# Performance work log

Measured on AMD Instinct MI355X. Metric: run time of the kernel, lower is better.

## Reference

```python
import jax, jax.numpy as jnp
from jax import lax
import numpy as np

T, B, D, H = 4096, 32, 512, 256


def setup_inputs() -> dict:
    key = jax.random.key(0)
    ks = jax.random.split(key, 8)
    s_ih = 1.0 / np.sqrt(H)
    inp = {
        "x": jax.random.normal(ks[0], (T, B, D), dtype=jnp.float32),
        "reset": jax.random.randint(ks[1], (T, B), 0, 2, dtype=jnp.int32),
        # PyTorch nn.LSTM params, gate order (i, f, g, o)
        "W_ih": jax.random.uniform(ks[2], (4 * H, D), jnp.float32, -s_ih, s_ih),
        "W_hh": jax.random.uniform(ks[3], (4 * H, H), jnp.float32, -s_ih, s_ih),
        "b_ih": jax.random.uniform(ks[4], (4 * H,), jnp.float32, -s_ih, s_ih),
        "b_hh": jax.random.uniform(ks[5], (4 * H,), jnp.float32, -s_ih, s_ih),
        "W_proj": jax.random.uniform(ks[6], (1, H), jnp.float32, -s_ih, s_ih),
        "b_proj": jax.random.uniform(ks[7], (1,), jnp.float32, -s_ih, s_ih),
    }
    return inp


def _lstm_with_reset(x, reset, W_ih, W_hh, b_ih, b_hh):
    # Precompute input contribution for all timesteps: [T, B, 4H]
    xW = jnp.einsum("tbd,gd->tbg", x, W_ih) + b_ih + b_hh
    h0 = jnp.zeros((x.shape[1], H), x.dtype)
    c0 = jnp.zeros((x.shape[1], H), x.dtype)

    def step(carry, inp):
        h, c = carry
        xw, r = inp
        keep = (1 - r).astype(h.dtype)[:, None]  # zero state at episode starts
        h = h * keep
        c = c * keep
        gates = xw + h @ W_hh.T  # [B, 4H]
        i, f, g, o = jnp.split(gates, 4, axis=-1)
        c = jax.nn.sigmoid(f) * c + jax.nn.sigmoid(i) * jnp.tanh(g)
        h = jax.nn.sigmoid(o) * jnp.tanh(c)
        return (h, c), h

    (_, _), hs = lax.scan(step, (h0, c0), (xW, reset))
    return hs  # [T, B, H]


def reference(x, reset, W_ih, W_hh, b_ih, b_hh, W_proj, b_proj):
    hs = _lstm_with_reset(x, reset, W_ih, W_hh, b_ih, b_hh)
    return hs @ W_proj.T + b_proj  # [T, B, 1]
```

## Files before the change

### kernel.cpp

```cpp
#include <hip/hip_runtime.h>
#include <cstdint>
#include <cstddef>

#define T_DIM 4096
#define B_DIM 32
#define D_DIM 512
#define H_DIM 256
#define G_DIM 1024
#define HSTR 264
#define XSTR 1036
#define NBUCK 64

typedef _Float16 h8 __attribute__((ext_vector_type(8)));
typedef float f4 __attribute__((ext_vector_type(4)));

__global__ void seg_build_kernel(const int* __restrict__ reset,
                                 unsigned* __restrict__ starts,
                                 unsigned* __restrict__ segcnt) {
  __shared__ unsigned cnts[256];
  __shared__ unsigned offs[256];
  const int b = blockIdx.x;
  const int tid = threadIdx.x;
  const int t0 = tid * 16;
  unsigned c = 0;
  for (int e = 0; e < 16; ++e) {
    int t = t0 + e;
    bool pred = (t == 0) || (reset[t * B_DIM + b] != 0);
    c += pred ? 1u : 0u;
  }
  cnts[tid] = c;
  __syncthreads();
  if (tid == 0) {
    unsigned run = 0;
    for (int i = 0; i < 256; ++i) { unsigned v = cnts[i]; offs[i] = run; run += v; }
    segcnt[b] = run;
  }
  __syncthreads();
  unsigned o = (unsigned)b * 4096u + offs[tid];
  for (int e = 0; e < 16; ++e) {
    int t = t0 + e;
    bool pred = (t == 0) || (reset[t * B_DIM + b] != 0);
    if (pred) { starts[o++] = (unsigned)t; }
  }
}

__global__ void seg_flat_kernel(const unsigned* __restrict__ starts,
                                const unsigned* __restrict__ segcnt,
                                uint2* __restrict__ flat2,
                                unsigned* __restrict__ meta) {
  __shared__ unsigned offs;
  const int b = blockIdx.x;
  const int tid = threadIdx.x;
  if (tid == 0) {
    unsigned o = 0;
    for (int i = 0; i < b; ++i) o += segcnt[i];
    offs = o;
    if (b == 31) meta[1] = o + segcnt[31];
    if (b == 0) meta[0] = 0u;
  }
  __syncthreads();
  const unsigned cnt = segcnt[b];
  const unsigned off = offs;
  for (unsigned s = tid; s < cnt; s += 256) {
    unsigned t0 = starts[b * 4096u + s];
    unsigned t1 = (s + 1 < cnt) ? starts[b * 4096u + s + 1] : 4096u;
    flat2[off + s] = make_uint2(t0 | ((unsigned)b << 16), t1);
  }
}

__global__ void seg_sort_kernel(const uint2* __restrict__ flat2,
                                uint2* __restrict__ flat,
                                const unsigned* __restrict__ meta) {
  __shared__ unsigned lh[NBUCK];
  __shared__ unsigned cur[NBUCK];
  const unsigned nseg = meta[1];
  const int tid = threadIdx.x;
  const int lane = tid & 63;
  if (tid < NBUCK) lh[tid] = 0u;
  __syncthreads();
  for (unsigned base = 0; base < nseg; base += 1024) {
    unsigned i = base + tid;
    bool act = i < nseg;
    unsigned bk = 0u;
    if (act) {
      uint2 e = flat2[i];
      bk = min(e.y - (e.x & 0xFFFFu), (unsigned)NBUCK) - 1u;
    }
    unsigned long long rem = __ballot(act);
    while (rem) {
      int ld = (int)__ffsll((unsigned long long)rem) - 1;
      unsigned lbk = __shfl(bk, ld);
      unsigned long long meq = __ballot(act && bk == lbk);
      if (lane == ld) atomicAdd(&lh[lbk], (unsigned)__popcll(meq));
      rem &= ~meq;
    }
  }
  __syncthreads();
  if (tid == 0) {
    unsigned run = 0;
    for (int k = NBUCK - 1; k >= 0; --k) { cur[k] = run; run += lh[k]; }
  }
  __syncthreads();
  for (unsigned base = 0; base < nseg; base += 1024) {
    unsigned i = base + tid;
    bool act = i < nseg;
    uint2 e = make_uint2(0u, 0u);
    unsigned bk = 0u;
    if (act) {
      e = flat2[i];
      bk = min(e.y - (e.x & 0xFFFFu), (unsigned)NBUCK) - 1u;
    }
    unsigned long long rem = __ballot(act);
    unsigned pos = 0u;
    while (rem) {
      int ld = (int)__ffsll((unsigned long long)rem) - 1;
      unsigned lbk = __shfl(bk, ld);
      unsigned long long meq = __ballot(act && bk == lbk);
      unsigned bs = 0u;
      if (lane == ld) bs = atomicAdd(&cur[lbk], (unsigned)__popcll(meq));
      bs = __shfl(bs, ld);
      if (act && bk == lbk)
        pos = bs + (unsigned)__popcll(meq & ((1ull << lane) - 1ull));
      rem &= ~meq;
    }
    if (act) flat[pos] = e;
  }
}

__global__ void wpack_kernel(const float* __restrict__ Whh,
                             _Float16* __restrict__ wpack) {
  int gid = blockIdx.x * 256 + threadIdx.x;
  int nt = gid >> 9;
  int rem = gid & 511;
  int ks = rem >> 6;
  int l = rem & 63;
  int n = nt * 16 + (l & 15);
  int k = ks * 32 + (l >> 4) * 8;
  const float* src = Whh + (size_t)n * H_DIM + k;
  f4 v0 = *(const f4*)src;
  f4 v1 = *(const f4*)(src + 4);
  h8 wv = {(_Float16)v0.x, (_Float16)v0.y, (_Float16)v0.z, (_Float16)v0.w,
           (_Float16)v1.x, (_Float16)v1.y, (_Float16)v1.z, (_Float16)v1.w};
  *(h8*)(wpack + (size_t)gid * 8) = wv;
}

#define BM 128
#define BN 128
#define BK 32

__global__ __launch_bounds__(256) void xw_gemm_kernel(
    const float* __restrict__ X, const float* __restrict__ Wih,
    const float* __restrict__ bih, const float* __restrict__ bhh,
    _Float16* __restrict__ xw) {
  __shared__ _Float16 As[BM * BK];
  __shared__ _Float16 Bs[BN * BK];
  const int tid = threadIdx.x;
  const int lane = tid & 63;
  const int wave = tid >> 6;
  const unsigned wg = blockIdx.x;
  const unsigned xcd = wg & 7u;
  const unsigned idx = wg >> 3;
  const size_t m0 = (size_t)(xcd * 128u + (idx >> 3)) * BM;
  const int n0 = (int)(idx & 7u) * BN;
  const int wm = (wave & 1) * 64;
  const int wn = (wave >> 1) * 64;
  const int q = lane >> 4;
  const int r = lane & 15;

  f4 acc[4][4];
#pragma unroll
  for (int i = 0; i < 4; ++i)
#pragma unroll
    for (int j = 0; j < 4; ++j) { f4 z = {0.f, 0.f, 0.f, 0.f}; acc[i][j] = z; }

  const int srow = tid >> 1;
  const int kh = (tid & 1) * 16;

  for (int k0 = 0; k0 < D_DIM; k0 += BK) {
    const float* ax = X + (m0 + (size_t)srow) * D_DIM + k0 + kh;
    const float* bx = Wih + ((size_t)(n0 + srow)) * D_DIM + k0 + kh;
    f4 a0 = *(const f4*)(ax);
    f4 a1 = *(const f4*)(ax + 4);
    f4 a2 = *(const f4*)(ax + 8);
    f4 a3 = *(const f4*)(ax + 12);
    f4 b0 = *(const f4*)(bx);
    f4 b1 = *(const f4*)(bx + 4);
    f4 b2 = *(const f4*)(bx + 8);
    f4 b3 = *(const f4*)(bx + 12);
    h8 ha0 = {(_Float16)a0.x, (_Float16)a0.y, (_Float16)a0.z, (_Float16)a0.w,
              (_Float16)a1.x, (_Float16)a1.y, (_Float16)a1.z, (_Float16)a1.w};
    h8 ha1 = {(_Float16)a2.x, (_Float16)a2.y, (_Float16)a2.z, (_Float16)a2.w,
              (_Float16)a3.x, (_Float16)a3.y, (_Float16)a3.z, (_Float16)a3.w};
    h8 hb0 = {(_Float16)b0.x, (_Float16)b0.y, (_Float16)b0.z, (_Float16)b0.w,
              (_Float16)b1.x, (_Float16)b1.y, (_Float16)b1.z, (_Float16)b1.w};
    h8 hb1 = {(_Float16)b2.x, (_Float16)b2.y, (_Float16)b2.z, (_Float16)b2.w,
              (_Float16)b3.x, (_Float16)b3.y, (_Float16)b3.z, (_Float16)b3.w};
    *(h8*)(As + srow * BK + kh) = ha0;
    *(h8*)(As + srow * BK + kh + 8) = ha1;
    *(h8*)(Bs + srow * BK + kh) = hb0;
    *(h8*)(Bs + srow * BK + kh + 8) = hb1;
    __syncthreads();

    h8 af[4], bf[4];
#pragma unroll
    for (int mi = 0; mi < 4; ++mi)
      af[mi] = *(const h8*)(As + (wm + mi * 16 + r) * BK + q * 8);
#pragma unroll
    for (int ni = 0; ni < 4; ++ni)
      bf[ni] = *(const h8*)(Bs + (wn + ni * 16 + r) * BK + q * 8);
#pragma unroll
    for (int mi = 0; mi < 4; ++mi)
#pragma unroll
      for (int ni = 0; ni < 4; ++ni)
        acc[mi][ni] = __builtin_amdgcn_mfma_f32_16x16x32_f16(af[mi], bf[ni], acc[mi][ni], 0, 0, 0);
    __syncthreads();
  }

#pragma unroll
  for (int mi = 0; mi < 4; ++mi) {
#pragma unroll
    for (int ni = 0; ni < 4; ++ni) {
      int n = n0 + wn + ni * 16 + r;
      float bias = bih[n] + bhh[n];
#pragma unroll
      for (int reg = 0; reg < 4; ++reg) {
        size_t m = m0 + (size_t)(wm + mi * 16 + q * 4 + reg);
        xw[m * G_DIM + n] = (_Float16)(acc[mi][ni][reg] + bias);
      }
    }
  }
}

__device__ __forceinline__ float sigmf(float x) {
  return __builtin_amdgcn_rcpf(1.f + __expf(-x));
}
__device__ __forceinline__ float tanhf_(float x) {
  return 2.f * __builtin_amdgcn_rcpf(1.f + __expf(-2.f * x)) - 1.f;
}
__device__ __forceinline__ f4 MF(h8 a, h8 b, f4 c) {
  return __builtin_amdgcn_mfma_f32_16x16x32_f16(a, b, c, 0, 0, 0);
}

#define WPKp(g, j, ks) \
  ((const h8*)(wpack + (((size_t)((((g)*16 + 2*w + (j)) * 8 + (ks))) * 64 + l) * 8)))
#define ARD(mt, ks) (*(const h8*)(Hbuf + (16*(mt) + r16) * HSTR + (ks)*32 + q*8))

#define MFK_REG(KS) do {                                                   \
  h8 a0_ = ARD(0, KS), a1_ = ARD(1, KS);                                   \
  _Pragma("unroll") for (int g = 0; g < 4; ++g)                            \
  _Pragma("unroll") for (int j = 0; j < 2; ++j) {                          \
    acc[0][g][j] = MF(a0_, wr[g][j][KS], acc[0][g][j]);                    \
    acc[1][g][j] = MF(a1_, wr[g][j][KS], acc[1][g][j]); }                  \
} while (0)

#define MFK_W2() do {                                                      \
  h8 a0_ = ARD(0, 2), a1_ = ARD(1, 2);                                     \
  _Pragma("unroll") for (int g = 0; g < 4; ++g)                            \
  _Pragma("unroll") for (int j = 0; j < 2; ++j) {                          \
    h8 b_ = *(const h8*)(Wlds + (size_t)((((g)*16 + 2*w + (j)) * 64 + l)) * 8); \
    acc[0][g][j] = MF(a0_, b_, acc[0][g][j]);                              \
    acc[1][g][j] = MF(a1_, b_, acc[1][g][j]); }                            \
} while (0)

#define MFK_S(BUF, KS) do {                                                \
  h8 a0_ = ARD(0, KS), a1_ = ARD(1, KS);                                   \
  _Pragma("unroll") for (int g = 0; g < 4; ++g)                            \
  _Pragma("unroll") for (int j = 0; j < 2; ++j) {                          \
    acc[0][g][j] = MF(a0_, BUF[g][j], acc[0][g][j]);                       \
    acc[1][g][j] = MF(a1_, BUF[g][j], acc[1][g][j]); }                     \
} while (0)

#define LOAD_S(BUF, KS) do {                                               \
  _Pragma("unroll") for (int g = 0; g < 4; ++g)                            \
  _Pragma("unroll") for (int j = 0; j < 2; ++j)                            \
    BUF[g][j] = *WPKp(g, j, KS);                                           \
} while (0)

#define XRD(MT, G, J) do {                                                 \
  f4 xv;                                                                   \
  int rb_ = 16*(MT) + q*4;                                                 \
  int nn_ = (G)*256 + w*32 + 16*(J) + r16;                                 \
  xv.x = (float)xwlds[(rb_+0)*XSTR + nn_];                                 \
  xv.y = (float)xwlds[(rb_+1)*XSTR + nn_];                                 \
  xv.z = (float)xwlds[(rb_+2)*XSTR + nn_];                                 \
  xv.w = (float)xwlds[(rb_+3)*XSTR + nn_];                                 \
  acc[MT][G][J] += xv; } while (0)

#define CONTROL_STEP do {                                                     \
  int m = tid;                                                                \
  bool aliv = alivef[m] != 0;                                                 \
  if (aliv) {                                                                 \
    unsigned oi = outix[m];                                                   \
    if (oi != 0xFFFFFFFFu) {                                                  \
      float s = bp;                                                           \
      _Pragma("unroll") for (int ww = 0; ww < 8; ++ww) s += pbuf[ww][m];      \
      __builtin_nontemporal_store(s, &out[oi]);                               \
    }                                                                         \
  }                                                                           \
  bool cont = aliv && (tcur[m] + 1 < tend[m]);                                \
  bool need = aliv && !cont;                                                  \
  unsigned long long bal = __ballot(need);                                    \
  if (cont) {                                                                 \
    int t = tcur[m] + 1;                                                      \
    tcur[m] = t; keepm[m] = 1.f;                                              \
    unsigned row = (unsigned)t * 32u + (unsigned)bcol[m];                     \
    trowB[m] = row * 2048u; outix[m] = row;                                   \
  }                                                                           \
  if (bal) {                                                                  \
    unsigned cntp = (unsigned)__popcll(bal);                                  \
    int ldr = (int)__ffsll(bal) - 1;                                          \
    unsigned basep = 0;                                                       \
    if ((tid & 63) == ldr) basep = atomicAdd(ctr, cntp);                      \
    basep = __shfl(basep, ldr);                                               \
    if (need) {                                                               \
      unsigned idx = basep +                                                  \
          (unsigned)__popcll(bal & ((1ull << (tid & 63)) - 1ull));            \
      if (idx < nseg) {                                                       \
        uint2 sg = flat[idx];                                                 \
        int t0s = (int)(sg.x & 0xFFFFu); int bb = (int)(sg.x >> 16);          \
        tcur[m] = t0s; tend[m] = (int)sg.y; bcol[m] = bb; keepm[m] = 0.f;     \
        unsigned row = (unsigned)t0s * 32u + (unsigned)bb;                    \
        trowB[m] = row * 2048u; outix[m] = row;                               \
        h8 zz = {0,0,0,0,0,0,0,0};                                            \
        _Pragma("unroll") for (int i2 = 0; i2 < 33; ++i2)                     \
          *(h8*)(Hbuf + (size_t)m * HSTR + i2 * 8) = zz;                      \
      } else {                                                                \
        alivef[m] = 0; outix[m] = 0xFFFFFFFFu; trowB[m] = 0;                  \
        keepm[m] = 0.f;                                                       \
      }                                                                       \
    }                                                                         \
  }                                                                           \
} while (0)

__global__ __launch_bounds__(512, 2) void lstm_scan_mfma(
    const _Float16* __restrict__ xw,
    const _Float16* __restrict__ wpack,
    const float* __restrict__ Wproj,
    const float* __restrict__ bproj,
    const uint2* __restrict__ flat,
    unsigned* __restrict__ meta,
    float* __restrict__ out) {
  __shared__ __align__(16) _Float16 Wlds[64 * 64 * 8];
  __shared__ __align__(16) _Float16 xwlds[32 * XSTR];
  __shared__ __align__(16) _Float16 Hbuf[32 * HSTR];
  __shared__ __align__(16) float pbuf[8][32];
  __shared__ __align__(16) unsigned trowB[32];
  __shared__ __align__(16) float keepm[32];
  __shared__ unsigned outix[32];
  __shared__ int tcur[32], tend[32], bcol[32], alivef[32];

  const int tid = threadIdx.x;
  const int l = tid & 63;
  const int w = tid >> 6;
  const int q = l >> 4;
  const int r16 = l & 15;
  const char* xwc = (const char*)xw;
  unsigned* ctr = meta;
  const unsigned nseg = meta[1];

  for (int it = 0; it < 16; ++it) {
    int idx = it * 512 + tid;
    int nt = idx >> 6;
    int ll = idx & 63;
    *(h8*)(Wlds + (size_t)idx * 8) =
        *(const h8*)(wpack + (((size_t)(nt * 8 + 2)) * 64 + ll) * 8);
  }
  for (int i = tid; i < 32 * HSTR / 8; i += 512) {
    h8 z = {0,0,0,0,0,0,0,0};
    *(h8*)(Hbuf + (size_t)i * 8) = z;
  }
  h8 wr[4][2][2];
#pragma unroll
  for (int g = 0; g < 4; ++g)
#pragma unroll
    for (int j = 0; j < 2; ++j)
#pragma unroll
      for (int ks = 0; ks < 2; ++ks)
        wr[g][j][ks] = *WPKp(g, j, ks);

  const float wpv0 = Wproj[32 * w + r16];
  const float wpv1 = Wproj[32 * w + 16 + r16];
  const float bp = bproj[0];
  if (tid < 32) {
    alivef[tid] = 1; tcur[tid] = 0; tend[tid] = 0; bcol[tid] = 0;
    outix[tid] = 0xFFFFFFFFu; trowB[tid] = 0; keepm[tid] = 0.f;
  }
  float cst[16];
#pragma unroll
  for (int i = 0; i < 16; ++i) cst[i] = 0.f;
  __syncthreads();
  if (tid < 32) CONTROL_STEP;
  int nalive = __syncthreads_count(tid < 32 ? alivef[tid] : 0);

  while (nalive > 0) {
#pragma unroll
    for (int rnd = 0; rnd < 8; ++rnd) {
      int c = rnd * 8 + w;
      unsigned rowB = trowB[c >> 1];
      const char* src = xwc + (size_t)rowB + (size_t)((c & 1) * 1024) + (size_t)l * 16;
      _Float16* dst = xwlds + (size_t)(c >> 1) * XSTR + (c & 1) * 512;
      __builtin_amdgcn_global_load_lds((const uint32_t*)src, (uint32_t*)dst, 16, 0, 0);
    }

    f4 z4 = {0.f, 0.f, 0.f, 0.f};
    f4 acc[2][4][2];
#pragma unroll
    for (int mt = 0; mt < 2; ++mt)
#pragma unroll
      for (int g = 0; g < 4; ++g)
#pragma unroll
        for (int j = 0; j < 2; ++j) acc[mt][g][j] = z4;
    h8 sA[4][2], sB[4][2];

    LOAD_S(sA, 3); LOAD_S(sB, 4);
    MFK_REG(0);
    MFK_REG(1);
    MFK_W2();
    MFK_S(sA, 3); LOAD_S(sA, 5);
    MFK_S(sB, 4); LOAD_S(sB, 6);
    MFK_S(sA, 5); LOAD_S(sA, 7);
    MFK_S(sB, 6);
    MFK_S(sA, 7);

    __syncthreads();

    XRD(0, 0, 0); XRD(0, 0, 1);
    XRD(0, 1, 0); XRD(0, 1, 1);
    XRD(0, 2, 0); XRD(0, 2, 1);
    XRD(0, 3, 0); XRD(0, 3, 1);
    XRD(1, 0, 0); XRD(1, 0, 1);
    XRD(1, 1, 0); XRD(1, 1, 1);
    XRD(1, 2, 0); XRD(1, 2, 1);
    XRD(1, 3, 0); XRD(1, 3, 1);

    f4 kp0 = *(const f4*)&keepm[q * 4];
    f4 kp1 = *(const f4*)&keepm[16 + q * 4];
    float pr[8];
#pragma unroll
    for (int r = 0; r < 4; ++r) {
      {
        float gi = sigmf(acc[0][0][0][r]);
        float gf = sigmf(acc[0][1][0][r]);
        float gg = tanhf_(acc[0][2][0][r]);
        float go = sigmf(acc[0][3][0][r]);
        float cn = gf * (cst[r] * kp0[r]) + gi * gg;
        cst[r] = cn;
        float hv = go * tanhf_(cn);
        Hbuf[(q * 4 + r) * HSTR + 32 * w + r16] = (_Float16)hv;
        pr[r] = hv * wpv0;
      }
      {
        float gi = sigmf(acc[0][0][1][r]);
        float gf = sigmf(acc[0][1][1][r]);
        float gg = tanhf_(acc[0][2][1][r]);
        float go = sigmf(acc[0][3][1][r]);
        float cn = gf * (cst[4 + r] * kp0[r]) + gi * gg;
        cst[4 + r] = cn;
        float hv = go * tanhf_(cn);
        Hbuf[(q * 4 + r) * HSTR + 32 * w + 16 + r16] = (_Float16)hv;
        pr[r] += hv * wpv1;
      }
    }
#pragma unroll
    for (int r = 0; r < 4; ++r) {
      {
        float gi = sigmf(acc[1][0][0][r]);
        float gf = sigmf(acc[1][1][0][r]);
        float gg = tanhf_(acc[1][2][0][r]);
        float go = sigmf(acc[1][3][0][r]);
        float cn = gf * (cst[8 + r] * kp1[r]) + gi * gg;
        cst[8 + r] = cn;
        float hv = go * tanhf_(cn);
        Hbuf[(16 + q * 4 + r) * HSTR + 32 * w + r16] = (_Float16)hv;
        pr[4 + r] = hv * wpv0;
      }
      {
        float gi = sigmf(acc[1][0][1][r]);
        float gf = sigmf(acc[1][1][1][r]);
        float gg = tanhf_(acc[1][2][1][r]);
        float go = sigmf(acc[1][3][1][r]);
        float cn = gf * (cst[12 + r] * kp1[r]) + gi * gg;
        cst[12 + r] = cn;
        float hv = go * tanhf_(cn);
        Hbuf[(16 + q * 4 + r) * HSTR + 32 * w + 16 + r16] = (_Float16)hv;
        pr[4 + r] += hv * wpv1;
      }
    }
#pragma unroll
    for (int jj = 0; jj < 8; ++jj) {
      pr[jj] += __shfl_xor(pr[jj], 1);
      pr[jj] += __shfl_xor(pr[jj], 2);
      pr[jj] += __shfl_xor(pr[jj], 4);
      pr[jj] += __shfl_xor(pr[jj], 8);
    }
    if (r16 == 0) {
#pragma unroll
      for (int jj = 0; jj < 8; ++jj)
        pbuf[w][16 * (jj >> 2) + q * 4 + (jj & 3)] = pr[jj];
    }

    __syncthreads();
    if (tid < 32) CONTROL_STEP;
    nalive = __syncthreads_count(tid < 32 ? alivef[tid] : 0);
  }
}

extern "C" void kernel_launch(void* const* d_in, const int* in_sizes, int n_in,
                              void* d_out, int out_size, void* d_ws, size_t ws_size,
                              hipStream_t stream) {
  const float* x = (const float*)d_in[0];
  const int* reset = (const int*)d_in[1];
  const float* Wih = (const float*)d_in[2];
  const float* Whh = (const float*)d_in[3];
  const float* bih = (const float*)d_in[4];
  const float* bhh = (const float*)d_in[5];
  const float* Wproj = (const float*)d_in[6];
  const float* bproj = (const float*)d_in[7];
  float* out = (float*)d_out;

  char* ws = (char*)d_ws;
  _Float16* xw = (_Float16*)ws;
  unsigned* starts = (unsigned*)(ws + 268435456ULL);
  unsigned* segcnt = (unsigned*)(ws + 268959744ULL);
  uint2* flat = (uint2*)(ws + 268959872ULL);
  _Float16* wpack = (_Float16*)(ws + 270008448ULL);
  unsigned* meta = (unsigned*)(ws + 270532736ULL);
  uint2* flat2 = (uint2*)ws;

  hipLaunchKernelGGL(seg_build_kernel, dim3(32), dim3(256), 0, stream,
                     reset, starts, segcnt);
  hipLaunchKernelGGL(seg_flat_kernel, dim3(32), dim3(256), 0, stream,
                     starts, segcnt, flat2, meta);
  hipLaunchKernelGGL(seg_sort_kernel, dim3(1), dim3(1024), 0, stream,
                     flat2, flat, meta);
  hipLaunchKernelGGL(wpack_kernel, dim3(128), dim3(256), 0, stream,
                     Whh, wpack);
  hipLaunchKernelGGL(xw_gemm_kernel, dim3(8192), dim3(256), 0, stream,
                     x, Wih, bih, bhh, xw);
  hipLaunchKernelGGL(lstm_scan_mfma, dim3(256), dim3(512), 0, stream,
                     xw, wpack, Wproj, bproj, flat, meta, out);
}
```

Before: 1.207 ms.

## Pre-convert X and W_ih to fp16 and use a direct-load MFMA input GEMM

Adds a pass that converts x to fp16 and a kernel that packs W_ih into MFMA fragment order. A new input GEMM then loads A/B fragments straight from global memory without LDS staging. This path is used only when the workspace is large enough. It also switches the scan kernel's launch attributes to explicit waves-per-EU and sets a cache-policy bit on the global-to-LDS loads. The goal is to halve input-GEMM read traffic and remove in-kernel conversion and LDS overhead, at the cost of an extra full pass over x and a large workspace.

```diff
diff --git a/kernel.cpp b/kernel.cpp
--- a/kernel.cpp
+++ b/kernel.cpp
@@ -144,9 +144,96 @@
   *(h8*)(wpack + (size_t)gid * 8) = wv;
 }
 
+__global__ __launch_bounds__(256) void xcvt_kernel(const float* __restrict__ X,
+                                                   _Float16* __restrict__ xh) {
+  const int n8 = (T_DIM * B_DIM * D_DIM) / 8;
+  int stride = gridDim.x * blockDim.x;
+  for (int i = blockIdx.x * blockDim.x + threadIdx.x; i < n8; i += stride) {
+    const float* s = X + (size_t)i * 8;
+    f4 a = *(const f4*)s;
+    f4 b = *(const f4*)(s + 4);
+    h8 v = {(_Float16)a.x, (_Float16)a.y, (_Float16)a.z, (_Float16)a.w,
+            (_Float16)b.x, (_Float16)b.y, (_Float16)b.z, (_Float16)b.w};
+    *(h8*)(xh + (size_t)i * 8) = v;
+  }
+}
+
+__global__ void wihpack_kernel(const float* __restrict__ Wih,
+                               _Float16* __restrict__ wihp) {
+  int gid = blockIdx.x * 256 + threadIdx.x;
+  int nt = gid >> 10;
+  int ks = (gid >> 6) & 15;
+  int l = gid & 63;
+  int n = nt * 16 + (l & 15);
+  int k = ks * 32 + (l >> 4) * 8;
+  const float* src = Wih + (size_t)n * D_DIM + k;
+  f4 v0 = *(const f4*)src;
+  f4 v1 = *(const f4*)(src + 4);
+  h8 wv = {(_Float16)v0.x, (_Float16)v0.y, (_Float16)v0.z, (_Float16)v0.w,
+           (_Float16)v1.x, (_Float16)v1.y, (_Float16)v1.z, (_Float16)v1.w};
+  *(h8*)(wihp + (size_t)gid * 8) = wv;
+}
+
 #define BM 128
 #define BN 128
 #define BK 32
+
+__global__ __launch_bounds__(256) void xw_gemm_direct(
+    const _Float16* __restrict__ xh, const _Float16* __restrict__ wihp,
+    const float* __restrict__ bih, const float* __restrict__ bhh,
+    _Float16* __restrict__ xw) {
+  const int tid = threadIdx.x;
+  const int lane = tid & 63;
+  const int wave = tid >> 6;
+  const unsigned wg = blockIdx.x;
+  const unsigned xcd = wg & 7u;
+  const unsigned idx = wg >> 3;
+  const size_t m0 = (size_t)(xcd * 128u + (idx >> 3)) * BM;
+  const int n0 = (int)(idx & 7u) * BN;
+  const int wm = (wave & 1) * 64;
+  const int wn = (wave >> 1) * 64;
+  const int q = lane >> 4;
+  const int r = lane & 15;
+
+  f4 acc[4][4];
+#pragma unroll
+  for (int i = 0; i < 4; ++i)
+#pragma unroll
+    for (int j = 0; j < 4; ++j) { f4 z = {0.f, 0.f, 0.f, 0.f}; acc[i][j] = z; }
+
+  const _Float16* aBase = xh + (m0 + (size_t)(wm + r)) * D_DIM + q * 8;
+  const _Float16* bBase = wihp + ((size_t)(((n0 + wn) >> 4) * 16) * 64 + lane) * 8;
+
+#pragma unroll 4
+  for (int ks = 0; ks < 16; ++ks) {
+    h8 af[4], bf[4];
+#pragma unroll
+    for (int mi = 0; mi < 4; ++mi)
+      af[mi] = *(const h8*)(aBase + (size_t)mi * (16 * D_DIM) + ks * 32);
+#pragma unroll
+    for (int ni = 0; ni < 4; ++ni)
+      bf[ni] = *(const h8*)(bBase + (size_t)(ni * 16 + ks) * (64 * 8));
+#pragma unroll
+    for (int mi = 0; mi < 4; ++mi)
+#pragma unroll
+      for (int ni = 0; ni < 4; ++ni)
+        acc[mi][ni] = __builtin_amdgcn_mfma_f32_16x16x32_f16(af[mi], bf[ni], acc[mi][ni], 0, 0, 0);
+  }
+
+#pragma unroll
+  for (int mi = 0; mi < 4; ++mi) {
+#pragma unroll
+    for (int ni = 0; ni < 4; ++ni) {
+      int n = n0 + wn + ni * 16 + r;
+      float bias = bih[n] + bhh[n];
+#pragma unroll
+      for (int reg = 0; reg < 4; ++reg) {
+        size_t m = m0 + (size_t)(wm + mi * 16 + q * 4 + reg);
+        xw[m * G_DIM + n] = (_Float16)(acc[mi][ni][reg] + bias);
+      }
+    }
+  }
+}
 
 __global__ __launch_bounds__(256) void xw_gemm_kernel(
     const float* __restrict__ X, const float* __restrict__ Wih,
@@ -332,7 +419,9 @@
   }                                                                           \
 } while (0)
 
-__global__ __launch_bounds__(512, 2) void lstm_scan_mfma(
+__global__ __attribute__((amdgpu_flat_work_group_size(512, 512),
+                          amdgpu_waves_per_eu(2, 2)))
+void lstm_scan_mfma(
     const _Float16* __restrict__ xw,
     const _Float16* __restrict__ wpack,
     const float* __restrict__ Wproj,
@@ -399,7 +488,7 @@
       unsigned rowB = trowB[c >> 1];
       const char* src = xwc + (size_t)rowB + (size_t)((c & 1) * 1024) + (size_t)l * 16;
       _Float16* dst = xwlds + (size_t)(c >> 1) * XSTR + (c & 1) * 512;
-      __builtin_amdgcn_global_load_lds((const uint32_t*)src, (uint32_t*)dst, 16, 0, 0);
+      __builtin_amdgcn_global_load_lds((const uint32_t*)src, (uint32_t*)dst, 16, 0, 2);
     }
 
     f4 z4 = {0.f, 0.f, 0.f, 0.f};
@@ -525,6 +614,9 @@
   uint2* flat = (uint2*)(ws + 268959872ULL);
   _Float16* wpack = (_Float16*)(ws + 270008448ULL);
   unsigned* meta = (unsigned*)(ws + 270532736ULL);
+  _Float16* xh = (_Float16*)(ws + 270532864ULL);
+  _Float16* wihp = (_Float16*)(ws + 404750592ULL);
+  const bool big = ws_size >= 405799168ULL;
   uint2* flat2 = (uint2*)ws;
 
   hipLaunchKernelGGL(seg_build_kernel, dim3(32), dim3(256), 0, stream,
@@ -535,8 +627,16 @@
                      flat2, flat, meta);
   hipLaunchKernelGGL(wpack_kernel, dim3(128), dim3(256), 0, stream,
                      Whh, wpack);
-  hipLaunchKernelGGL(xw_gemm_kernel, dim3(8192), dim3(256), 0, stream,
-                     x, Wih, bih, bhh, xw);
+  if (big) {
+    hipLaunchKernelGGL(xcvt_kernel, dim3(2048), dim3(256), 0, stream, x, xh);
+    hipLaunchKernelGGL(wihpack_kernel, dim3(256), dim3(256), 0, stream,
+                       Wih, wihp);
+    hipLaunchKernelGGL(xw_gemm_direct, dim3(8192), dim3(256), 0, stream,
+                       xh, wihp, bih, bhh, xw);
+  } else {
+    hipLaunchKernelGGL(xw_gemm_kernel, dim3(8192), dim3(256), 0, stream,
+                       x, Wih, bih, bhh, xw);
+  }
   hipLaunchKernelGGL(lstm_scan_mfma, dim3(256), dim3(512), 0, stream,
                      xw, wpack, Wproj, bproj, flat, meta, out);
 }
```

After: 1.318 ms. 9.2% more time.
